# Kernel optimization log

Hardware: AMD Instinct MI355X
Metric: run time of the kernel (lower is better)

Reference implementation:

```python
import jax, jax.numpy as jnp
import numpy as np

N_USERS = 100000
N_ITEMS = 50000
N_NODES = N_USERS + N_ITEMS
LATENT = 64
NNZ = 2400000
BATCH = 2048
EPS = 1e-12  # F.normalize eps


def setup_inputs() -> dict:
    key = jax.random.key(0)
    ks = jax.random.split(key, 16)
    inp = {
        "rows": jax.random.randint(ks[0], (NNZ,), 0, N_NODES, dtype=jnp.int32),
        "cols": jax.random.randint(ks[1], (NNZ,), 0, N_NODES, dtype=jnp.int32),
        "vals": jax.random.uniform(ks[2], (NNZ,), dtype=jnp.float32),
        "x": jax.random.normal(ks[3], (N_NODES, LATENT), dtype=jnp.float32) * 0.1,
        "users": jax.random.randint(ks[12], (BATCH,), 0, N_USERS, dtype=jnp.int32),
        "items": jax.random.randint(ks[13], (BATCH,), 0, N_ITEMS, dtype=jnp.int32),
    }
    for k in range(2):
        inp[f"W_gc{k}"] = jax.random.normal(ks[4 + 4 * k], (LATENT, LATENT), dtype=jnp.float32) * 0.1
        inp[f"b_gc{k}"] = jax.random.normal(ks[5 + 4 * k], (1, LATENT), dtype=jnp.float32) * 0.1
        inp[f"W_bi{k}"] = jax.random.normal(ks[6 + 4 * k], (LATENT, LATENT), dtype=jnp.float32) * 0.1
        inp[f"b_bi{k}"] = jax.random.normal(ks[7 + 4 * k], (1, LATENT), dtype=jnp.float32) * 0.1
    return inp


def _l2_normalize(v):
    # F.normalize(p=2, dim=1): divide by max(||v||_2, eps)
    n = jnp.sqrt(jnp.sum(v * v, axis=1, keepdims=True))
    return v / jnp.maximum(n, EPS)


def reference(rows, cols, vals, x,
              W_gc0, b_gc0, W_bi0, b_bi0,
              W_gc1, b_gc1, W_bi1, b_bi1,
              users, items):
    weights = [(W_gc0, b_gc0, W_bi0, b_bi0), (W_gc1, b_gc1, W_bi1, b_bi1)]
    ego = x                      # [N, D]
    embs = [x]
    for (Wg, bg, Wb, bb) in weights:
        # sparse adj @ ego  (COO gather + segment-sum scatter)
        msgs = vals[:, None] * ego[cols]                              # [nnz, D]
        side = jax.ops.segment_sum(msgs, rows, num_segments=N_NODES)  # [N, D]
        sum_emb = side @ Wg + bg
        bi_emb = (ego * side) @ Wb + bb
        ego = _l2_normalize(jax.nn.leaky_relu(sum_emb + bi_emb, negative_slope=0.2))
        embs.append(ego)
    all_emb = jnp.concatenate(embs, axis=1)          # [N, 3*D]
    users_emb = all_emb[users]                       # [B, 3*D]
    items_emb = all_emb[N_USERS + items]             # [B, 3*D]
    gamma = jnp.sum(users_emb * items_emb, axis=1)   # [B]
    return gamma
```

## Files before the change

kernel.cpp:

```cpp
#include <hip/hip_runtime.h>

#define N_USERS_C 100000
#define N_NODES_C 150000
#define D 64
#define NB 2344
#define NSUP 74
#define CPAD 16
#define SPAD 68
#define FCAP 1536
#define S1B 256
#define FRAG 240
#define S2CAP 2560
#define BPS 16
#define FPB (S1B / BPS)
#define NSCAN 147
#define MARK 1

__global__ __launch_bounds__(256) void mark1_k(
    const int* __restrict__ u, const int* __restrict__ it,
    unsigned char* __restrict__ samp, unsigned char* __restrict__ need, int batch)
{
    int i = blockIdx.x * blockDim.x + threadIdx.x;
    if (i >= 2 * batch) return;
    int n = (i < batch) ? u[i] : N_USERS_C + it[i - batch];
    samp[n] = MARK;
    need[n] = MARK;
}

__global__ __launch_bounds__(256) void mark2_k(
    const int* __restrict__ rows, const int* __restrict__ cols,
    const unsigned char* __restrict__ samp, unsigned char* __restrict__ need, int nnz)
{
    int gtid = blockIdx.x * blockDim.x + threadIdx.x;
    int stride = gridDim.x * blockDim.x;
    for (int e = gtid; e < nnz; e += stride)
        if (samp[rows[e]] == MARK) need[cols[e]] = MARK;
}

__global__ __launch_bounds__(1024) void scan1_k(
    const unsigned char* __restrict__ need, int* __restrict__ part,
    int* __restrict__ bsum, int n)
{
    __shared__ int wsum[16];
    int i = blockIdx.x * 1024 + threadIdx.x;
    int lane = threadIdx.x & 63, wid = threadIdx.x >> 6;
    int v = (i < n && need[i] == MARK) ? 1 : 0;
    int incl = v;
    #pragma unroll
    for (int off = 1; off < 64; off <<= 1) {
        int t = __shfl_up(incl, off);
        if (lane >= off) incl += t;
    }
    if (lane == 63) wsum[wid] = incl;
    __syncthreads();
    int woff = 0;
    for (int w = 0; w < wid; ++w) woff += wsum[w];
    if (i < n) part[i] = woff + incl - v;
    if (threadIdx.x == 1023) bsum[blockIdx.x] = woff + incl;
}

__global__ __launch_bounds__(256) void scanB_k(
    const int* __restrict__ bsum, int* __restrict__ idx,
    const unsigned char* __restrict__ need, int* __restrict__ list,
    int* __restrict__ bcur, int* __restrict__ Mptr, int n)
{
    __shared__ int pre[NSCAN + 1];
    __shared__ int raw[NSCAN];
    int t = threadIdx.x;
    if (t < NSCAN) raw[t] = bsum[t];
    __syncthreads();
    if (t == 0) {
        int run = 0;
        for (int k = 0; k < NSCAN; ++k) { pre[k] = run; run += raw[k]; }
        pre[NSCAN] = run;
    }
    __syncthreads();
    int i = blockIdx.x * blockDim.x + t;
    if (i < NB) bcur[i * CPAD] = i * FCAP;
    if (blockIdx.x == 0 && t == 0) Mptr[0] = pre[NSCAN];
    if (i >= n) return;
    int val = idx[i] + pre[i >> 10];
    if (need[i] == MARK) { idx[i] = val; list[val] = i; }
    else idx[i] = -1;
}

__global__ __launch_bounds__(512) void s1_k(
    const int* __restrict__ rows, const int* __restrict__ cols,
    const float* __restrict__ vals, const int* __restrict__ idx,
    int2* __restrict__ pairs1, int* __restrict__ scnt, int nnz)
{
    __shared__ int lcur[NSUP];
    int t = threadIdx.x;
    for (int i = t; i < NSUP; i += 512) lcur[i] = 0;
    __syncthreads();
    int b = blockIdx.x;
    int per = (nnz + S1B - 1) / S1B;
    int s = b * per;
    int e = min(nnz, s + per);
    for (int i = s + t; i < e; i += 512) {
        int ci = idx[rows[i]];
        if (ci < 0) continue;
        int sp = ci >> 11;
        int k = atomicAdd(&lcur[sp], 1);
        pairs1[(size_t)sp * (S1B * FRAG) + b * FRAG + k] =
            make_int2(((ci & 2047) << 18) | cols[i], __float_as_int(vals[i]));
    }
    __syncthreads();
    for (int i = t; i < NSUP; i += 512) scnt[i * S1B + b] = lcur[i];
}

__global__ __launch_bounds__(256) void s2_k(
    const int* __restrict__ scnt, const int2* __restrict__ pairs1,
    int* __restrict__ bcurP, int2* __restrict__ pairs)
{
    __shared__ int2 sbuf[S2CAP];
    __shared__ int fcnt[32], fcur[32], gb[32];
    int sp = blockIdx.x / BPS, part = blockIdx.x % BPS;
    int t = threadIdx.x;
    if (t < 32) { fcnt[t] = 0; fcur[t] = 0; }
    __syncthreads();
    int base = 0;
    for (int fi = 0; fi < FPB; ++fi) {
        int b = part * FPB + fi;
        int m = scnt[sp * S1B + b];
        const int2* src = &pairs1[(size_t)sp * (S1B * FRAG) + b * FRAG];
        for (int i = t; i < m; i += 256) {
            int2 p = src[i];
            sbuf[base + i] = p;
            atomicAdd(&fcnt[(p.x >> 18) >> 6], 1);
        }
        base += m;
    }
    __syncthreads();
    if (t < 32) {
        int c = fcnt[t];
        gb[t] = c ? atomicAdd(&bcurP[(sp * 32 + t) * CPAD], c) : 0;
    }
    __syncthreads();
    for (int i = t; i < base; i += 256) {
        int2 p = sbuf[i];
        int ris = p.x >> 18;
        int f = ris >> 6;
        int k = atomicAdd(&fcur[f], 1);
        pairs[gb[f] + k] = make_int2(((ris & 63) << 18) | (p.x & 0x3FFFF), p.y);
    }
}

__global__ __launch_bounds__(256) void sortb_k(
    const int* __restrict__ bcurP, int2* __restrict__ pairs,
    int* __restrict__ rp)
{
    __shared__ int2 buf[FCAP];
    __shared__ int cnt[64];
    __shared__ int cur[64];
    int b = blockIdx.x;
    int s = b * FCAP;
    int e = bcurP[b * CPAD];
    int m = e - s;
    int t = threadIdx.x;
    if (t < 64) cnt[t] = 0;
    __syncthreads();
    for (int i = t; i < m; i += 256) {
        int2 p = pairs[s + i];
        buf[i] = p;
        atomicAdd(&cnt[p.x >> 18], 1);
    }
    __syncthreads();
    if (t < 64) {
        int v = cnt[t];
        int incl = v;
        #pragma unroll
        for (int o = 1; o < 64; o <<= 1) {
            int u = __shfl_up(incl, o);
            if (t >= o) incl += u;
        }
        cur[t] = incl - v;
        rp[b * 65 + t] = s + incl - v;
        if (t == 63) rp[b * 65 + 64] = s + incl;
    }
    __syncthreads();
    for (int i = t; i < m; i += 256) {
        int2 p = buf[i];
        int dst = atomicAdd(&cur[p.x >> 18], 1);
        pairs[s + dst] = make_int2(p.x & 0x3FFFF, p.y);
    }
}

__global__ __launch_bounds__(256) void gather1_k(
    const int* __restrict__ rp, const int2* __restrict__ pairs,
    const float* __restrict__ x, float* __restrict__ side,
    const int* __restrict__ Mptr)
{
    int gtid = blockIdx.x * blockDim.x + threadIdx.x;
    int wave = gtid >> 6;
    int lane = threadIdx.x & 63;
    int M = Mptr[0];
    if (wave * 4 >= M) return;
    int lq = lane & 15;
    int qb = lane & 48;
    int row = wave * 4 + (lane >> 4);
    int valid = row < M;
    int s = 0, len = 0;
    if (valid) {
        int rb = (row >> 6) * 65 + (row & 63);
        s = rp[rb];
        len = rp[rb + 1] - s;
    }
    int ml = len;
    ml = max(ml, __shfl_xor(ml, 16));
    ml = max(ml, __shfl_xor(ml, 32));

    float4 acc = make_float4(0.f, 0.f, 0.f, 0.f);
    for (int base = 0; base < ml; base += 16) {
        int2 p = make_int2(0, 0);
        int o = base + lq;
        if (o < len) p = pairs[s + o];
        int rem = len - base;
        rem = min(max(rem, 0), 16);
        int mr = rem;
        mr = max(mr, __shfl_xor(mr, 16));
        mr = max(mr, __shfl_xor(mr, 32));
        int cnt8 = (mr + 7) & ~7;
        for (int j = 0; j < cnt8; j += 8) {
            int c[8]; float v[8]; float4 f[8];
            #pragma unroll
            for (int q = 0; q < 8; ++q) {
                c[q] = __shfl(p.x, qb | (j + q));
                v[q] = __int_as_float(__shfl(p.y, qb | (j + q)));
            }
            #pragma unroll
            for (int q = 0; q < 8; ++q)
                f[q] = *(const float4*)&x[(size_t)c[q] * D + lq * 4];
            #pragma unroll
            for (int q = 0; q < 8; ++q) {
                acc.x = fmaf(v[q], f[q].x, acc.x);
                acc.y = fmaf(v[q], f[q].y, acc.y);
                acc.z = fmaf(v[q], f[q].z, acc.z);
                acc.w = fmaf(v[q], f[q].w, acc.w);
            }
        }
    }
    if (valid) *(float4*)&side[(size_t)row * D + lq * 4] = acc;
}

__global__ __launch_bounds__(256) void gather2_k(
    const int* __restrict__ rp, const int2* __restrict__ pairs,
    const float* __restrict__ e1c, const int* __restrict__ idx,
    float* __restrict__ side2c, float* __restrict__ egoc,
    const int* __restrict__ u, const int* __restrict__ it, int batch)
{
    int gtid = blockIdx.x * blockDim.x + threadIdx.x;
    int wave = gtid >> 6;
    int lane = threadIdx.x & 63;
    int nr = 2 * batch;
    if (wave * 4 >= nr) return;
    int lq = lane & 15;
    int qb = lane & 48;
    int r = wave * 4 + (lane >> 4);
    int valid = r < nr;
    int s = 0, len = 0, cr = 0;
    if (valid) {
        int n = (r < batch) ? u[r] : N_USERS_C + it[r - batch];
        cr = idx[n];
        int rb = (cr >> 6) * 65 + (cr & 63);
        s = rp[rb];
        len = rp[rb + 1] - s;
    }
    int ml = len;
    ml = max(ml, __shfl_xor(ml, 16));
    ml = max(ml, __shfl_xor(ml, 32));

    float4 acc = make_float4(0.f, 0.f, 0.f, 0.f);
    for (int base = 0; base < ml; base += 16) {
        int2 p = make_int2(0, 0);
        int o = base + lq;
        if (o < len) p = pairs[s + o];
        int rem = len - base;
        rem = min(max(rem, 0), 16);
        int mr = rem;
        mr = max(mr, __shfl_xor(mr, 16));
        mr = max(mr, __shfl_xor(mr, 32));
        int cnt8 = (mr + 7) & ~7;
        for (int j = 0; j < cnt8; j += 8) {
            int c[8]; float v[8]; float4 f[8];
            #pragma unroll
            for (int q = 0; q < 8; ++q) {
                c[q] = __shfl(p.x, qb | (j + q));
                v[q] = __int_as_float(__shfl(p.y, qb | (j + q)));
            }
            #pragma unroll
            for (int q = 0; q < 8; ++q) {
                int cc = idx[c[q]];
                cc = max(cc, 0);
                f[q] = *(const float4*)&e1c[(size_t)cc * D + lq * 4];
            }
            #pragma unroll
            for (int q = 0; q < 8; ++q) {
                acc.x = fmaf(v[q], f[q].x, acc.x);
                acc.y = fmaf(v[q], f[q].y, acc.y);
                acc.z = fmaf(v[q], f[q].z, acc.z);
                acc.w = fmaf(v[q], f[q].w, acc.w);
            }
        }
    }
    if (valid) {
        *(float4*)&side2c[(size_t)r * D + lq * 4] = acc;
        *(float4*)&egoc[(size_t)r * D + lq * 4] =
            *(const float4*)&e1c[(size_t)cr * D + lq * 4];
    }
}

__global__ __launch_bounds__(256) void transform_k(
    const float* __restrict__ S, const float* __restrict__ Eb,
    const float* __restrict__ Wg, const float* __restrict__ bg,
    const float* __restrict__ Wb, const float* __restrict__ bb,
    float* __restrict__ out, const int* __restrict__ list,
    const int* __restrict__ Mptr, int nrows)
{
    __shared__ __align__(16) float sWg[D * D];
    __shared__ __align__(16) float sWb[D * D];
    __shared__ __align__(16) float sAT[D][SPAD];
    __shared__ __align__(16) float sBT[D][SPAD];

    int nr = Mptr ? Mptr[0] : nrows;
    int t  = threadIdx.x;
    int tc = t & 15;
    int tr = t >> 4;
    int r0 = blockIdx.x * 64;
    if (r0 >= nr) return;

    for (int i = t; i < D * D; i += 256) {
        sWg[i] = Wg[i];
        sWb[i] = Wb[i];
    }
    for (int itr = 0; itr < 4; ++itr) {
        int rr  = itr * 16 + (t >> 4);
        int row = r0 + rr;
        float4 sv = make_float4(0.f, 0.f, 0.f, 0.f);
        float4 ev = sv;
        if (row < nr) {
            sv = *(const float4*)&S[(size_t)row * D + tc * 4];
            int er = list ? list[row] : row;
            ev = *(const float4*)&Eb[(size_t)er * D + tc * 4];
        }
        sAT[tc * 4 + 0][rr] = sv.x;
        sAT[tc * 4 + 1][rr] = sv.y;
        sAT[tc * 4 + 2][rr] = sv.z;
        sAT[tc * 4 + 3][rr] = sv.w;
        sBT[tc * 4 + 0][rr] = sv.x * ev.x;
        sBT[tc * 4 + 1][rr] = sv.y * ev.y;
        sBT[tc * 4 + 2][rr] = sv.z * ev.z;
        sBT[tc * 4 + 3][rr] = sv.w * ev.w;
    }
    __syncthreads();

    float acc[4][4] = {};
    for (int k = 0; k < D; ++k) {
        float4 a4 = *(const float4*)&sAT[k][tr * 4];
        float4 b4 = *(const float4*)&sBT[k][tr * 4];
        float4 g4 = *(const float4*)&sWg[k * D + tc * 4];
        float4 w4 = *(const float4*)&sWb[k * D + tc * 4];
        float av[4] = {a4.x, a4.y, a4.z, a4.w};
        float bv[4] = {b4.x, b4.y, b4.z, b4.w};
        float gv[4] = {g4.x, g4.y, g4.z, g4.w};
        float wv[4] = {w4.x, w4.y, w4.z, w4.w};
        #pragma unroll
        for (int i = 0; i < 4; ++i)
            #pragma unroll
            for (int j = 0; j < 4; ++j)
                acc[i][j] = fmaf(av[i], gv[j], fmaf(bv[i], wv[j], acc[i][j]));
    }

    float4 bgv = *(const float4*)&bg[tc * 4];
    float4 bbv = *(const float4*)&bb[tc * 4];
    float bias[4] = {bgv.x + bbv.x, bgv.y + bbv.y, bgv.z + bbv.z, bgv.w + bbv.w};

    float vv[4][4];
    float ss[4] = {0.f, 0.f, 0.f, 0.f};
    #pragma unroll
    for (int i = 0; i < 4; ++i) {
        #pragma unroll
        for (int j = 0; j < 4; ++j) {
            float v = acc[i][j] + bias[j];
            v = (v > 0.0f) ? v : 0.2f * v;
            vv[i][j] = v;
            ss[i] += v * v;
        }
    }
    #pragma unroll
    for (int i = 0; i < 4; ++i) {
        #pragma unroll
        for (int off = 1; off < 16; off <<= 1)
            ss[i] += __shfl_xor(ss[i], off);
    }
    #pragma unroll
    for (int i = 0; i < 4; ++i) {
        int row = r0 + tr * 4 + i;
        if (row < nr) {
            float inv = 1.0f / fmaxf(sqrtf(ss[i]), 1e-12f);
            float4 o = make_float4(vv[i][0] * inv, vv[i][1] * inv,
                                   vv[i][2] * inv, vv[i][3] * inv);
            *(float4*)&out[(size_t)row * D + tc * 4] = o;
        }
    }
}

__global__ __launch_bounds__(256) void gamma_k(
    const float* __restrict__ x, const float* __restrict__ e1c,
    const int* __restrict__ idx, const float* __restrict__ e2c,
    const int* __restrict__ users, const int* __restrict__ items,
    float* __restrict__ gamma, int batch)
{
    int gtid = blockIdx.x * blockDim.x + threadIdx.x;
    int wave = gtid >> 6;
    int lane = threadIdx.x & 63;
    if (wave >= batch) return;
    size_t uu = (size_t)users[wave];
    size_t tt = (size_t)(N_USERS_C + items[wave]);
    float acc = x[uu * D + lane] * x[tt * D + lane]
              + e1c[(size_t)idx[uu] * D + lane] * e1c[(size_t)idx[tt] * D + lane]
              + e2c[(size_t)wave * D + lane] * e2c[(size_t)(batch + wave) * D + lane];
    #pragma unroll
    for (int off = 1; off < 64; off <<= 1) acc += __shfl_xor(acc, off);
    if (lane == 0) gamma[wave] = acc;
}

extern "C" void kernel_launch(void* const* d_in, const int* in_sizes, int n_in,
                              void* d_out, int out_size, void* d_ws, size_t ws_size,
                              hipStream_t stream) {
    const int*   rows  = (const int*)d_in[0];
    const int*   cols  = (const int*)d_in[1];
    const float* vals  = (const float*)d_in[2];
    const float* x     = (const float*)d_in[3];
    const int*   users = (const int*)d_in[4];
    const int*   items = (const int*)d_in[5];
    const float* Wg0 = (const float*)d_in[6];
    const float* bg0 = (const float*)d_in[7];
    const float* Wb0 = (const float*)d_in[8];
    const float* bb0 = (const float*)d_in[9];
    const float* Wg1 = (const float*)d_in[10];
    const float* bg1 = (const float*)d_in[11];
    const float* Wb1 = (const float*)d_in[12];
    const float* bb1 = (const float*)d_in[13];

    int nnz   = in_sizes[0];
    int batch = in_sizes[4];
    float* out = (float*)d_out;

    size_t emb = (size_t)N_NODES_C * D;
    float* A      = (float*)d_ws;
    float* Sbuf   = A + emb;
    int*   bcur   = (int*)(Sbuf + emb);
    int*   rp     = bcur + NB * CPAD;
    int*   idx    = rp + NB * 65 + 2;
    int*   list   = idx + N_NODES_C;
    int*   bsum   = list + N_NODES_C;
    int*   Mptr   = bsum + 1024;
    int*   scnt   = Mptr + 4;
    unsigned char* need = (unsigned char*)(scnt + NSUP * S1B);
    unsigned char* samp = need + N_NODES_C;
    int2*  pairs  = (int2*)(((size_t)(samp + N_NODES_C) + 15) & ~(size_t)15);

    int2*  pairs1 = (int2*)Sbuf;
    float* side2c = Sbuf;
    float* egoc   = Sbuf + (size_t)2 * 2048 * D;
    float* e2c    = egoc + (size_t)2 * 2048 * D;

    mark1_k<<<(2 * batch + 255) / 256, 256, 0, stream>>>(users, items, samp, need, batch);
    mark2_k<<<1024, 256, 0, stream>>>(rows, cols, samp, need, nnz);
    scan1_k<<<NSCAN, 1024, 0, stream>>>(need, idx, bsum, N_NODES_C);
    scanB_k<<<(N_NODES_C + 255) / 256, 256, 0, stream>>>(bsum, idx, need, list, bcur, Mptr, N_NODES_C);

    s1_k<<<S1B, 512, 0, stream>>>(rows, cols, vals, idx, pairs1, scnt, nnz);
    s2_k<<<NSUP * BPS, 256, 0, stream>>>(scnt, pairs1, bcur, pairs);
    sortb_k<<<NB, 256, 0, stream>>>(bcur, pairs, rp);

    gather1_k<<<(N_NODES_C / 4 * 64 + 255) / 256, 256, 0, stream>>>(
        rp, pairs, x, Sbuf, Mptr);
    transform_k<<<(N_NODES_C + 63) / 64, 256, 0, stream>>>(
        Sbuf, x, Wg0, bg0, Wb0, bb0, A, list, Mptr, 0);

    gather2_k<<<(2 * batch / 4 * 64 + 255) / 256, 256, 0, stream>>>(
        rp, pairs, A, idx, side2c, egoc, users, items, batch);
    transform_k<<<(2 * batch + 63) / 64, 256, 0, stream>>>(
        side2c, egoc, Wg1, bg1, Wb1, bb1, e2c, nullptr, nullptr, 2 * batch);

    gamma_k<<<(batch * 64 + 255) / 256, 256, 0, stream>>>(
        x, A, idx, e2c, users, items, out, batch);
}
```

Baseline: 251.4 us.

## Fuse sparse gather with dense transform for both GCN layers

Merges each gather kernel with its following transform kernel. The aggregated neighbour sums are written straight into shared-memory transposed tiles instead of round-tripping through a global side buffer, which removes two launches and the global write and read of the intermediate. The weight matrices are now read from global/L1 instead of being staged in LDS, and launch_bounds requests higher occupancy. The tradeoff is that each block now does the irregular gather before the matmul, so load imbalance inside a block can stall the dense phase.

```diff
diff --git a/kernel.cpp b/kernel.cpp
--- a/kernel.cpp
+++ b/kernel.cpp
@@ -186,180 +186,94 @@
     }
 }
 
-__global__ __launch_bounds__(256) void gather1_k(
+__global__ __launch_bounds__(256, 4) void fuse1_k(
     const int* __restrict__ rp, const int2* __restrict__ pairs,
-    const float* __restrict__ x, float* __restrict__ side,
-    const int* __restrict__ Mptr)
-{
-    int gtid = blockIdx.x * blockDim.x + threadIdx.x;
-    int wave = gtid >> 6;
-    int lane = threadIdx.x & 63;
-    int M = Mptr[0];
-    if (wave * 4 >= M) return;
-    int lq = lane & 15;
-    int qb = lane & 48;
-    int row = wave * 4 + (lane >> 4);
-    int valid = row < M;
-    int s = 0, len = 0;
-    if (valid) {
-        int rb = (row >> 6) * 65 + (row & 63);
-        s = rp[rb];
-        len = rp[rb + 1] - s;
-    }
-    int ml = len;
-    ml = max(ml, __shfl_xor(ml, 16));
-    ml = max(ml, __shfl_xor(ml, 32));
-
-    float4 acc = make_float4(0.f, 0.f, 0.f, 0.f);
-    for (int base = 0; base < ml; base += 16) {
-        int2 p = make_int2(0, 0);
-        int o = base + lq;
-        if (o < len) p = pairs[s + o];
-        int rem = len - base;
-        rem = min(max(rem, 0), 16);
-        int mr = rem;
-        mr = max(mr, __shfl_xor(mr, 16));
-        mr = max(mr, __shfl_xor(mr, 32));
-        int cnt8 = (mr + 7) & ~7;
-        for (int j = 0; j < cnt8; j += 8) {
-            int c[8]; float v[8]; float4 f[8];
-            #pragma unroll
-            for (int q = 0; q < 8; ++q) {
-                c[q] = __shfl(p.x, qb | (j + q));
-                v[q] = __int_as_float(__shfl(p.y, qb | (j + q)));
-            }
-            #pragma unroll
-            for (int q = 0; q < 8; ++q)
-                f[q] = *(const float4*)&x[(size_t)c[q] * D + lq * 4];
-            #pragma unroll
-            for (int q = 0; q < 8; ++q) {
-                acc.x = fmaf(v[q], f[q].x, acc.x);
-                acc.y = fmaf(v[q], f[q].y, acc.y);
-                acc.z = fmaf(v[q], f[q].z, acc.z);
-                acc.w = fmaf(v[q], f[q].w, acc.w);
-            }
-        }
-    }
-    if (valid) *(float4*)&side[(size_t)row * D + lq * 4] = acc;
-}
-
-__global__ __launch_bounds__(256) void gather2_k(
-    const int* __restrict__ rp, const int2* __restrict__ pairs,
-    const float* __restrict__ e1c, const int* __restrict__ idx,
-    float* __restrict__ side2c, float* __restrict__ egoc,
-    const int* __restrict__ u, const int* __restrict__ it, int batch)
-{
-    int gtid = blockIdx.x * blockDim.x + threadIdx.x;
-    int wave = gtid >> 6;
-    int lane = threadIdx.x & 63;
-    int nr = 2 * batch;
-    if (wave * 4 >= nr) return;
-    int lq = lane & 15;
-    int qb = lane & 48;
-    int r = wave * 4 + (lane >> 4);
-    int valid = r < nr;
-    int s = 0, len = 0, cr = 0;
-    if (valid) {
-        int n = (r < batch) ? u[r] : N_USERS_C + it[r - batch];
-        cr = idx[n];
-        int rb = (cr >> 6) * 65 + (cr & 63);
-        s = rp[rb];
-        len = rp[rb + 1] - s;
-    }
-    int ml = len;
-    ml = max(ml, __shfl_xor(ml, 16));
-    ml = max(ml, __shfl_xor(ml, 32));
-
-    float4 acc = make_float4(0.f, 0.f, 0.f, 0.f);
-    for (int base = 0; base < ml; base += 16) {
-        int2 p = make_int2(0, 0);
-        int o = base + lq;
-        if (o < len) p = pairs[s + o];
-        int rem = len - base;
-        rem = min(max(rem, 0), 16);
-        int mr = rem;
-        mr = max(mr, __shfl_xor(mr, 16));
-        mr = max(mr, __shfl_xor(mr, 32));
-        int cnt8 = (mr + 7) & ~7;
-        for (int j = 0; j < cnt8; j += 8) {
-            int c[8]; float v[8]; float4 f[8];
-            #pragma unroll
-            for (int q = 0; q < 8; ++q) {
-                c[q] = __shfl(p.x, qb | (j + q));
-                v[q] = __int_as_float(__shfl(p.y, qb | (j + q)));
-            }
-            #pragma unroll
-            for (int q = 0; q < 8; ++q) {
-                int cc = idx[c[q]];
-                cc = max(cc, 0);
-                f[q] = *(const float4*)&e1c[(size_t)cc * D + lq * 4];
-            }
-            #pragma unroll
-            for (int q = 0; q < 8; ++q) {
-                acc.x = fmaf(v[q], f[q].x, acc.x);
-                acc.y = fmaf(v[q], f[q].y, acc.y);
-                acc.z = fmaf(v[q], f[q].z, acc.z);
-                acc.w = fmaf(v[q], f[q].w, acc.w);
-            }
-        }
-    }
-    if (valid) {
-        *(float4*)&side2c[(size_t)r * D + lq * 4] = acc;
-        *(float4*)&egoc[(size_t)r * D + lq * 4] =
-            *(const float4*)&e1c[(size_t)cr * D + lq * 4];
-    }
-}
-
-__global__ __launch_bounds__(256) void transform_k(
-    const float* __restrict__ S, const float* __restrict__ Eb,
+    const float* __restrict__ x,
     const float* __restrict__ Wg, const float* __restrict__ bg,
     const float* __restrict__ Wb, const float* __restrict__ bb,
     float* __restrict__ out, const int* __restrict__ list,
-    const int* __restrict__ Mptr, int nrows)
-{
-    __shared__ __align__(16) float sWg[D * D];
-    __shared__ __align__(16) float sWb[D * D];
+    const int* __restrict__ Mptr)
+{
     __shared__ __align__(16) float sAT[D][SPAD];
     __shared__ __align__(16) float sBT[D][SPAD];
 
-    int nr = Mptr ? Mptr[0] : nrows;
-    int t  = threadIdx.x;
+    int nr = Mptr[0];
+    int r0 = blockIdx.x * 64;
+    if (r0 >= nr) return;
+
+    int t    = threadIdx.x;
+    int lane = t & 63;
+    int wid  = t >> 6;
+    int lq   = lane & 15;
+    int qb   = lane & 48;
+
+    for (int pass = 0; pass < 4; ++pass) {
+        int rr  = wid * 16 + pass * 4 + (lane >> 4);
+        int row = r0 + rr;
+        int valid = row < nr;
+        int s = 0, len = 0, er = 0;
+        if (valid) {
+            int rb = (row >> 6) * 65 + (row & 63);
+            s = rp[rb];
+            len = rp[rb + 1] - s;
+            er = list[row];
+        }
+        int ml = len;
+        ml = max(ml, __shfl_xor(ml, 16));
+        ml = max(ml, __shfl_xor(ml, 32));
+
+        float4 acc = make_float4(0.f, 0.f, 0.f, 0.f);
+        for (int base = 0; base < ml; base += 16) {
+            int2 p = make_int2(0, 0);
+            int o = base + lq;
+            if (o < len) p = pairs[s + o];
+            int rem = len - base;
+            rem = min(max(rem, 0), 16);
+            int mr = rem;
+            mr = max(mr, __shfl_xor(mr, 16));
+            mr = max(mr, __shfl_xor(mr, 32));
+            int cnt8 = (mr + 7) & ~7;
+            for (int j = 0; j < cnt8; j += 8) {
+                int c[8]; float v[8]; float4 f[8];
+                #pragma unroll
+                for (int q = 0; q < 8; ++q) {
+                    c[q] = __shfl(p.x, qb | (j + q));
+                    v[q] = __int_as_float(__shfl(p.y, qb | (j + q)));
+                }
+                #pragma unroll
+                for (int q = 0; q < 8; ++q)
+                    f[q] = *(const float4*)&x[(size_t)c[q] * D + lq * 4];
+                #pragma unroll
+                for (int q = 0; q < 8; ++q) {
+                    acc.x = fmaf(v[q], f[q].x, acc.x);
+                    acc.y = fmaf(v[q], f[q].y, acc.y);
+                    acc.z = fmaf(v[q], f[q].z, acc.z);
+                    acc.w = fmaf(v[q], f[q].w, acc.w);
+                }
+            }
+        }
+        float4 ev = make_float4(0.f, 0.f, 0.f, 0.f);
+        if (valid) ev = *(const float4*)&x[(size_t)er * D + lq * 4];
+        sAT[lq * 4 + 0][rr] = acc.x;
+        sAT[lq * 4 + 1][rr] = acc.y;
+        sAT[lq * 4 + 2][rr] = acc.z;
+        sAT[lq * 4 + 3][rr] = acc.w;
+        sBT[lq * 4 + 0][rr] = acc.x * ev.x;
+        sBT[lq * 4 + 1][rr] = acc.y * ev.y;
+        sBT[lq * 4 + 2][rr] = acc.z * ev.z;
+        sBT[lq * 4 + 3][rr] = acc.w * ev.w;
+    }
+    __syncthreads();
+
     int tc = t & 15;
     int tr = t >> 4;
-    int r0 = blockIdx.x * 64;
-    if (r0 >= nr) return;
-
-    for (int i = t; i < D * D; i += 256) {
-        sWg[i] = Wg[i];
-        sWb[i] = Wb[i];
-    }
-    for (int itr = 0; itr < 4; ++itr) {
-        int rr  = itr * 16 + (t >> 4);
-        int row = r0 + rr;
-        float4 sv = make_float4(0.f, 0.f, 0.f, 0.f);
-        float4 ev = sv;
-        if (row < nr) {
-            sv = *(const float4*)&S[(size_t)row * D + tc * 4];
-            int er = list ? list[row] : row;
-            ev = *(const float4*)&Eb[(size_t)er * D + tc * 4];
-        }
-        sAT[tc * 4 + 0][rr] = sv.x;
-        sAT[tc * 4 + 1][rr] = sv.y;
-        sAT[tc * 4 + 2][rr] = sv.z;
-        sAT[tc * 4 + 3][rr] = sv.w;
-        sBT[tc * 4 + 0][rr] = sv.x * ev.x;
-        sBT[tc * 4 + 1][rr] = sv.y * ev.y;
-        sBT[tc * 4 + 2][rr] = sv.z * ev.z;
-        sBT[tc * 4 + 3][rr] = sv.w * ev.w;
-    }
-    __syncthreads();
-
-    float acc[4][4] = {};
+    float acc2[4][4] = {};
+    #pragma unroll 4
     for (int k = 0; k < D; ++k) {
         float4 a4 = *(const float4*)&sAT[k][tr * 4];
         float4 b4 = *(const float4*)&sBT[k][tr * 4];
-        float4 g4 = *(const float4*)&sWg[k * D + tc * 4];
-        float4 w4 = *(const float4*)&sWb[k * D + tc * 4];
+        float4 g4 = *(const float4*)&Wg[k * D + tc * 4];
+        float4 w4 = *(const float4*)&Wb[k * D + tc * 4];
         float av[4] = {a4.x, a4.y, a4.z, a4.w};
         float bv[4] = {b4.x, b4.y, b4.z, b4.w};
         float gv[4] = {g4.x, g4.y, g4.z, g4.w};
@@ -368,7 +282,7 @@
         for (int i = 0; i < 4; ++i)
             #pragma unroll
             for (int j = 0; j < 4; ++j)
-                acc[i][j] = fmaf(av[i], gv[j], fmaf(bv[i], wv[j], acc[i][j]));
+                acc2[i][j] = fmaf(av[i], gv[j], fmaf(bv[i], wv[j], acc2[i][j]));
     }
 
     float4 bgv = *(const float4*)&bg[tc * 4];
@@ -381,7 +295,144 @@
     for (int i = 0; i < 4; ++i) {
         #pragma unroll
         for (int j = 0; j < 4; ++j) {
-            float v = acc[i][j] + bias[j];
+            float v = acc2[i][j] + bias[j];
+            v = (v > 0.0f) ? v : 0.2f * v;
+            vv[i][j] = v;
+            ss[i] += v * v;
+        }
+    }
+    #pragma unroll
+    for (int i = 0; i < 4; ++i) {
+        #pragma unroll
+        for (int off = 1; off < 16; off <<= 1)
+            ss[i] += __shfl_xor(ss[i], off);
+    }
+    #pragma unroll
+    for (int i = 0; i < 4; ++i) {
+        int row = r0 + tr * 4 + i;
+        if (row < nr) {
+            float inv = 1.0f / fmaxf(sqrtf(ss[i]), 1e-12f);
+            float4 o = make_float4(vv[i][0] * inv, vv[i][1] * inv,
+                                   vv[i][2] * inv, vv[i][3] * inv);
+            *(float4*)&out[(size_t)row * D + tc * 4] = o;
+        }
+    }
+}
+
+__global__ __launch_bounds__(256, 4) void fuse2_k(
+    const int* __restrict__ rp, const int2* __restrict__ pairs,
+    const float* __restrict__ e1c, const int* __restrict__ idx,
+    const float* __restrict__ Wg, const float* __restrict__ bg,
+    const float* __restrict__ Wb, const float* __restrict__ bb,
+    float* __restrict__ out, const int* __restrict__ u,
+    const int* __restrict__ it, int batch)
+{
+    __shared__ __align__(16) float sAT[D][SPAD];
+    __shared__ __align__(16) float sBT[D][SPAD];
+
+    int nr = 2 * batch;
+    int r0 = blockIdx.x * 64;
+    if (r0 >= nr) return;
+
+    int t    = threadIdx.x;
+    int lane = t & 63;
+    int wid  = t >> 6;
+    int lq   = lane & 15;
+    int qb   = lane & 48;
+
+    for (int pass = 0; pass < 4; ++pass) {
+        int rr  = wid * 16 + pass * 4 + (lane >> 4);
+        int row = r0 + rr;
+        int valid = row < nr;
+        int s = 0, len = 0, cr = 0;
+        if (valid) {
+            int n = (row < batch) ? u[row] : N_USERS_C + it[row - batch];
+            cr = idx[n];
+            int rb = (cr >> 6) * 65 + (cr & 63);
+            s = rp[rb];
+            len = rp[rb + 1] - s;
+        }
+        int ml = len;
+        ml = max(ml, __shfl_xor(ml, 16));
+        ml = max(ml, __shfl_xor(ml, 32));
+
+        float4 acc = make_float4(0.f, 0.f, 0.f, 0.f);
+        for (int base = 0; base < ml; base += 16) {
+            int2 p = make_int2(0, 0);
+            int o = base + lq;
+            if (o < len) p = pairs[s + o];
+            int rem = len - base;
+            rem = min(max(rem, 0), 16);
+            int mr = rem;
+            mr = max(mr, __shfl_xor(mr, 16));
+            mr = max(mr, __shfl_xor(mr, 32));
+            int cnt8 = (mr + 7) & ~7;
+            for (int j = 0; j < cnt8; j += 8) {
+                int c[8]; float v[8]; float4 f[8];
+                #pragma unroll
+                for (int q = 0; q < 8; ++q) {
+                    c[q] = __shfl(p.x, qb | (j + q));
+                    v[q] = __int_as_float(__shfl(p.y, qb | (j + q)));
+                }
+                #pragma unroll
+                for (int q = 0; q < 8; ++q) {
+                    int cc = idx[c[q]];
+                    cc = max(cc, 0);
+                    f[q] = *(const float4*)&e1c[(size_t)cc * D + lq * 4];
+                }
+                #pragma unroll
+                for (int q = 0; q < 8; ++q) {
+                    acc.x = fmaf(v[q], f[q].x, acc.x);
+                    acc.y = fmaf(v[q], f[q].y, acc.y);
+                    acc.z = fmaf(v[q], f[q].z, acc.z);
+                    acc.w = fmaf(v[q], f[q].w, acc.w);
+                }
+            }
+        }
+        float4 ev = make_float4(0.f, 0.f, 0.f, 0.f);
+        if (valid) ev = *(const float4*)&e1c[(size_t)cr * D + lq * 4];
+        sAT[lq * 4 + 0][rr] = acc.x;
+        sAT[lq * 4 + 1][rr] = acc.y;
+        sAT[lq * 4 + 2][rr] = acc.z;
+        sAT[lq * 4 + 3][rr] = acc.w;
+        sBT[lq * 4 + 0][rr] = acc.x * ev.x;
+        sBT[lq * 4 + 1][rr] = acc.y * ev.y;
+        sBT[lq * 4 + 2][rr] = acc.z * ev.z;
+        sBT[lq * 4 + 3][rr] = acc.w * ev.w;
+    }
+    __syncthreads();
+
+    int tc = t & 15;
+    int tr = t >> 4;
+    float acc2[4][4] = {};
+    #pragma unroll 4
+    for (int k = 0; k < D; ++k) {
+        float4 a4 = *(const float4*)&sAT[k][tr * 4];
+        float4 b4 = *(const float4*)&sBT[k][tr * 4];
+        float4 g4 = *(const float4*)&Wg[k * D + tc * 4];
+        float4 w4 = *(const float4*)&Wb[k * D + tc * 4];
+        float av[4] = {a4.x, a4.y, a4.z, a4.w};
+        float bv[4] = {b4.x, b4.y, b4.z, b4.w};
+        float gv[4] = {g4.x, g4.y, g4.z, g4.w};
+        float wv[4] = {w4.x, w4.y, w4.z, w4.w};
+        #pragma unroll
+        for (int i = 0; i < 4; ++i)
+            #pragma unroll
+            for (int j = 0; j < 4; ++j)
+                acc2[i][j] = fmaf(av[i], gv[j], fmaf(bv[i], wv[j], acc2[i][j]));
+    }
+
+    float4 bgv = *(const float4*)&bg[tc * 4];
+    float4 bbv = *(const float4*)&bb[tc * 4];
+    float bias[4] = {bgv.x + bbv.x, bgv.y + bbv.y, bgv.z + bbv.z, bgv.w + bbv.w};
+
+    float vv[4][4];
+    float ss[4] = {0.f, 0.f, 0.f, 0.f};
+    #pragma unroll
+    for (int i = 0; i < 4; ++i) {
+        #pragma unroll
+        for (int j = 0; j < 4; ++j) {
+            float v = acc2[i][j] + bias[j];
             v = (v > 0.0f) ? v : 0.2f * v;
             vv[i][j] = v;
             ss[i] += v * v;
@@ -462,9 +513,7 @@
     int2*  pairs  = (int2*)(((size_t)(samp + N_NODES_C) + 15) & ~(size_t)15);
 
     int2*  pairs1 = (int2*)Sbuf;
-    float* side2c = Sbuf;
-    float* egoc   = Sbuf + (size_t)2 * 2048 * D;
-    float* e2c    = egoc + (size_t)2 * 2048 * D;
+    float* e2c    = Sbuf;
 
     mark1_k<<<(2 * batch + 255) / 256, 256, 0, stream>>>(users, items, samp, need, batch);
     mark2_k<<<1024, 256, 0, stream>>>(rows, cols, samp, need, nnz);
@@ -475,15 +524,11 @@
     s2_k<<<NSUP * BPS, 256, 0, stream>>>(scnt, pairs1, bcur, pairs);
     sortb_k<<<NB, 256, 0, stream>>>(bcur, pairs, rp);
 
-    gather1_k<<<(N_NODES_C / 4 * 64 + 255) / 256, 256, 0, stream>>>(
-        rp, pairs, x, Sbuf, Mptr);
-    transform_k<<<(N_NODES_C + 63) / 64, 256, 0, stream>>>(
-        Sbuf, x, Wg0, bg0, Wb0, bb0, A, list, Mptr, 0);
-
-    gather2_k<<<(2 * batch / 4 * 64 + 255) / 256, 256, 0, stream>>>(
-        rp, pairs, A, idx, side2c, egoc, users, items, batch);
-    transform_k<<<(2 * batch + 63) / 64, 256, 0, stream>>>(
-        side2c, egoc, Wg1, bg1, Wb1, bb1, e2c, nullptr, nullptr, 2 * batch);
+    fuse1_k<<<(N_NODES_C + 63) / 64, 256, 0, stream>>>(
+        rp, pairs, x, Wg0, bg0, Wb0, bb0, A, list, Mptr);
+
+    fuse2_k<<<(2 * batch + 63) / 64, 256, 0, stream>>>(
+        rp, pairs, A, idx, Wg1, bg1, Wb1, bb1, e2c, users, items, batch);
 
     gamma_k<<<(batch * 64 + 255) / 256, 256, 0, stream>>>(
         x, A, idx, e2c, users, items, out, batch);
```

New measurement: 256.0 us. About the same (+1.8%).
